# Performance work log

Measured on AMD Instinct MI355X. Metric: run time of the kernel, lower is better.

## Reference

```python
import jax, jax.numpy as jnp
import numpy as np
from jax import lax

S = 20      # max_segments
D = 1000    # traj_dict entries
L = 200     # dmp_traj_length
CONV_OUT = 512 * 4 * 4  # 8192 for 100x100 input


def _conv(x, w, b):
    # NCHW valid conv, kernel 3x3, stride 1 (matches nn.Conv2d defaults)
    y = lax.conv_general_dilated(x, w, (1, 1), 'VALID',
                                 dimension_numbers=('NCHW', 'OIHW', 'NCHW'))
    return y + b[None, :, None, None]


def _pool2(x):
    # max_pool2d(kernel=2, stride=2), floor mode == VALID reduce_window
    return lax.reduce_window(x, -jnp.inf, lax.max, (1, 1, 2, 2), (1, 1, 2, 2), 'VALID')


def setup_inputs() -> dict:
    key = jax.random.key(0)
    ks = jax.random.split(key, 20)
    f32 = jnp.float32

    def rn(k, shape, s):
        return jax.random.normal(k, shape, dtype=f32) * s

    x = jax.random.normal(ks[0], (128, 3, 100, 100), dtype=f32)
    w1 = rn(ks[1], (64, 3, 3, 3), 0.1);    b1 = jnp.zeros((64,), f32)
    w2 = rn(ks[2], (128, 64, 3, 3), 0.04); b2 = jnp.zeros((128,), f32)
    w3 = rn(ks[3], (256, 128, 3, 3), 0.03); b3 = jnp.zeros((256,), f32)
    w4 = rn(ks[4], (512, 256, 3, 3), 0.02); b4 = jnp.zeros((512,), f32)
    out_size = 2 + 3 * S
    fw1 = rn(ks[5], (CONV_OUT, 2048), 0.01); fb1 = jnp.zeros((2048,), f32)
    fw2 = rn(ks[6], (2048, 2048), 0.02);     fb2 = jnp.zeros((2048,), f32)
    fw3 = rn(ks[7], (2048, out_size), 0.02); fb3 = jnp.zeros((out_size,), f32)
    traj_dict = jax.random.normal(ks[8], (D, L, 2), dtype=f32)
    return {
        'x': x,
        'w1': w1, 'b1': b1, 'w2': w2, 'b2': b2,
        'w3': w3, 'b3': b3, 'w4': w4, 'b4': b4,
        'fw1': fw1, 'fb1': fb1, 'fw2': fw2, 'fb2': fb2,
        'fw3': fw3, 'fb3': fb3,
        'traj_dict': traj_dict,
    }


def _forward(x, w1, b1, w2, b2, w3, b3, w4, b4,
             fw1, fb1, fw2, fb2, fw3, fb3, traj_dict):
    # conv encoder (relu(maxpool(conv)) x4, matching the torch order)
    h = jax.nn.relu(_pool2(_conv(x, w1, b1)))
    h = jax.nn.relu(_pool2(_conv(h, w2, b2)))
    h = jax.nn.relu(_pool2(_conv(h, w3, b3)))
    h = jax.nn.relu(_pool2(_conv(h, w4, b4)))
    h = h.reshape(h.shape[0], -1)                      # [B, 8192]
    # FC stack: tanh on hidden layers, linear head (dropout p=0 / eval)
    h = jnp.tanh(h @ fw1 + fb1)
    h = jnp.tanh(h @ fw2 + fb2)
    p = h @ fw3 + fb3                                  # [B, 2 + 3S]

    B = p.shape[0]
    init_pos = p[:, :2]                                # [B, 2]
    seg = p[:, 2:].reshape(B, S, 3)                    # (dict_idx, x_scale, y_scale)

    # getTrajFromDict: the loop of round/clamp/sign/abs one-hot masks is exactly
    # a gather at the clamped rounded index (round is half-to-even in both torch and jax)
    idx = jnp.clip(jnp.round(seg[..., 0]), 0, D - 1).astype(jnp.int32)  # [B, S]
    base = traj_dict[idx]                              # [B, S, L, 2]

    scaled = base * seg[:, :, None, 1:3]               # [B, S, L, 2]
    # chain segments: each segment starts at previous segment's endpoint
    offsets = scaled[:, :, -1, :]                      # [B, S, 2]
    starts = init_pos[:, None, :] + jnp.cumsum(offsets, axis=1) - offsets  # exclusive cumsum
    traj = (scaled + starts[:, :, None, :]).reshape(B, S * L, 2)
    return traj


def reference(x, w1, b1, w2, b2, w3, b3, w4, b4,
              fw1, fb1, fw2, fb2, fw3, fb3, traj_dict):
    return _forward(x, w1, b1, w2, b2, w3, b3, w4, b4,
                    fw1, fb1, fw2, fb2, fw3, fb3, traj_dict)
```

## Files before the change

kernel.cpp:

```cpp
#include <hip/hip_runtime.h>
#include <hip/hip_bf16.h>

typedef __attribute__((ext_vector_type(8))) short s8v;
typedef __attribute__((ext_vector_type(4))) float f4v;
typedef unsigned short ushort;
typedef unsigned int uint;

union V8 { s8v v; short s[8]; };

__device__ __forceinline__ short f2bf(float v){
    union { __hip_bfloat16 b; short u; } x;
    x.b = __float2bfloat16(v);
    return x.u;
}
__device__ __forceinline__ float bf2f(short u){
    union { short u; __hip_bfloat16 b; } x;
    x.u = u;
    return __bfloat162float(x.b);
}
__device__ __forceinline__ void splitf(float v, short& h, short& l){
    h = f2bf(v);
    l = f2bf(v - bf2f(h));
}

__device__ __forceinline__ void gl_lds16(const void* g, void* l){
    __builtin_amdgcn_global_load_lds(
        (const __attribute__((address_space(1))) void*)g,
        (__attribute__((address_space(3))) void*)l, 16, 0, 0);
}

template<int CIN, int HIN, int PH, int OCB, int SPT, int CICH, int COUT>
__global__ __launch_bounds__(SPT) void k_conv_pool_relu(
    const float* __restrict__ in, const float* __restrict__ w,
    const float* __restrict__ bias, ushort* __restrict__ outh,
    ushort* __restrict__ outl)
{
    constexpr int WIN   = HIN;
    constexpr int PW    = PH;
    constexpr int WSTR  = CICH * 9 + 1;

    __shared__ float wsh[OCB * WSTR];

    const int b   = blockIdx.z;
    const int oc0 = blockIdx.y * OCB;
    const int t   = threadIdx.x;
    const int sp  = blockIdx.x * SPT + t;
    const bool active = sp < PH * PW;
    const int py = active ? (sp / PW) : 0;
    const int px = active ? (sp % PW) : 0;

    float acc[OCB][4];
#pragma unroll
    for (int j = 0; j < OCB; ++j)
        acc[j][0] = acc[j][1] = acc[j][2] = acc[j][3] = 0.f;

    const float* inb = in + (size_t)b * CIN * HIN * WIN;

    for (int c0 = 0; c0 < CIN; c0 += CICH) {
        __syncthreads();
        for (int i = t; i < OCB * CICH * 9; i += SPT) {
            int j = i / (CICH * 9);
            int r = i - j * (CICH * 9);
            wsh[j * WSTR + r] = w[((size_t)(oc0 + j) * CIN + c0) * 9 + r];
        }
        __syncthreads();

        for (int ci = 0; ci < CICH; ++ci) {
            const float* inc = inb + (size_t)(c0 + ci) * HIN * WIN
                             + (2 * py) * WIN + 2 * px;
            float patch[4][4];
#pragma unroll
            for (int r = 0; r < 4; ++r)
#pragma unroll
                for (int c = 0; c < 4; ++c)
                    patch[r][c] = inc[r * WIN + c];

#pragma unroll
            for (int j = 0; j < OCB; ++j) {
                const float* wp = &wsh[j * WSTR + ci * 9];
#pragma unroll
                for (int kh = 0; kh < 3; ++kh)
#pragma unroll
                    for (int kw = 0; kw < 3; ++kw) {
                        float wv = wp[kh * 3 + kw];
                        acc[j][0] = fmaf(patch[kh][kw],         wv, acc[j][0]);
                        acc[j][1] = fmaf(patch[kh][kw + 1],     wv, acc[j][1]);
                        acc[j][2] = fmaf(patch[kh + 1][kw],     wv, acc[j][2]);
                        acc[j][3] = fmaf(patch[kh + 1][kw + 1], wv, acc[j][3]);
                    }
            }
        }
    }

    if (active) {
        union { ushort us[OCB]; uint4 u4[OCB / 8]; } TH, TL;
#pragma unroll
        for (int j = 0; j < OCB; ++j) {
            float m = fmaxf(fmaxf(acc[j][0], acc[j][1]),
                            fmaxf(acc[j][2], acc[j][3]));
            m = fmaxf(m + bias[oc0 + j], 0.f);
            short h, l; splitf(m, h, l);
            TH.us[j] = (ushort)h; TL.us[j] = (ushort)l;
        }
        size_t base = ((size_t)b * PH * PW + sp) * COUT + oc0;
#pragma unroll
        for (int q = 0; q < OCB / 8; ++q) {
            ((uint4*)(outh + base))[q] = TH.u4[q];
            ((uint4*)(outl + base))[q] = TL.u4[q];
        }
    }
}

__global__ void k_wsplit_perm(const float* __restrict__ w, ushort* __restrict__ oh,
                              ushort* __restrict__ ol, int CIN, int total)
{
    int i = blockIdx.x * 256 + threadIdx.x;
    if (i < total) {
        int K = CIN * 9;
        int n = i / K;
        int rem = i - n * K;
        int ci = rem / 9;
        int r = rem - 9 * ci;
        short h, l; splitf(w[i], h, l);
        size_t o = (size_t)n * K + r * CIN + ci;
        oh[o] = (ushort)h; ol[o] = (ushort)l;
    }
}

__global__ __launch_bounds__(256) void k_wsplitT(
    const float* __restrict__ B, ushort* __restrict__ oh, ushort* __restrict__ ol,
    int K, int N)
{
    __shared__ float tl[32][33];
    const int n0 = blockIdx.x * 32, k0 = blockIdx.y * 32;
    const int r = threadIdx.x >> 5, c = threadIdx.x & 31;
#pragma unroll
    for (int it = 0; it < 4; ++it) {
        int row = r + it * 8;
        tl[row][c] = B[(size_t)(k0 + row) * N + n0 + c];
    }
    __syncthreads();
#pragma unroll
    for (int it = 0; it < 4; ++it) {
        int a = r + it * 8;
        float v = tl[c][a];
        short h, l; splitf(v, h, l);
        size_t o = (size_t)(n0 + a) * K + k0 + c;
        oh[o] = (ushort)h; ol[o] = (ushort)l;
    }
}

template<int MODE, int BPRE, int EPI, int LOG2CIN, int K, int KCH, int N,
         int HIN, int PPH, int PPW, int COUT, int TPI, int MT>
__global__ __launch_bounds__(256) void k_gemm4(
    const void* __restrict__ A0, const void* __restrict__ A1,
    const void* __restrict__ B0, const void* __restrict__ B1,
    const float* __restrict__ bias, void* __restrict__ O0, void* __restrict__ O1)
{
    constexpr int CIN  = 1 << LOG2CIN;
    constexpr int HH   = HIN * HIN;
    constexpr int WM   = MT / 32;
    constexpr int AOPT = MT / 64;
    constexpr int OSTEP = 256 / MT;

    __shared__ ushort Ah[4][MT][8], Al[4][MT][8];
    __shared__ ushort Bh[4][128][8], Bl[4][128][8];

    const int t    = threadIdx.x;
    const int lane = t & 63;
    const int wave = t >> 6;
    const int n0   = blockIdx.y * 128;
    const int sArow = t & (MT - 1), sAo0 = t / MT;
    const int sBrow = t & 127, sBo = t >> 7;
    const int rbA = sArow - lane;
    const int rbB = sBrow - lane;

    const ushort* Ahp = (const ushort*)A0;
    const ushort* Alp = (const ushort*)A1;
    size_t aoff = 0;
    const ushort* Ahg = nullptr;
    const ushort* Alg = nullptr;
    int b = 0, ptile = 0, kbeg = 0, kend = K;

    if (MODE == 0) {
        b = blockIdx.x / TPI;
        ptile = blockIdx.x - b * TPI;
        int pl = ptile * (MT / 4) + (sArow >> 2);
        int quad = sArow & 3;
        int py = 0, px = 0;
        if (pl < PPH * PPW) { py = pl / PPW; px = pl - py * PPW; }
        aoff = ((size_t)b * HH + (size_t)(2 * py + (quad >> 1)) * HIN
               + (2 * px + (quad & 1))) * CIN;
    } else {
        int arow = blockIdx.x * MT + sArow;
        Ahg = (const ushort*)A0 + (size_t)arow * K;
        Alg = (const ushort*)A1 + (size_t)arow * K;
        kbeg = blockIdx.z * KCH;
        kend = kbeg + KCH;
    }

    auto stage = [&](int kkx) {
#pragma unroll
        for (int q = 0; q < AOPT; ++q) {
            const int ko = sAo0 + q * OSTEP;
            const int kb = kkx + ko * 8;
            if (MODE == 0) {
                const int r  = kb >> LOG2CIN;
                const int cb = kb & (CIN - 1);
                const int rh = (r * 11) >> 5;
                const int rw = r - 3 * rh;
                const size_t g = aoff + (size_t)(rh * HIN + rw) * CIN + cb;
                gl_lds16(Ahp + g, &Ah[ko][rbA][0]);
                gl_lds16(Alp + g, &Al[ko][rbA][0]);
            } else {
                gl_lds16(Ahg + kb, &Ah[ko][rbA][0]);
                gl_lds16(Alg + kb, &Al[ko][rbA][0]);
            }
        }
        if (BPRE) {
#pragma unroll
            for (int q = 0; q < 2; ++q) {
                const int o = sBo + 2 * q;
                const int kb = kkx + o * 8;
                const size_t g = (size_t)(n0 + sBrow) * K + kb;
                gl_lds16((const ushort*)B0 + g, &Bh[o][rbB][0]);
                gl_lds16((const ushort*)B1 + g, &Bl[o][rbB][0]);
            }
        } else {
#pragma unroll
            for (int q = 0; q < 2; ++q) {
                const int o = sBo + 2 * q;
                const int kb = kkx + o * 8;
                V8 hb, lb;
                if (MODE == 0) {
                    const int r  = kb >> LOG2CIN;
                    const int cb = kb & (CIN - 1);
                    const float* bp = (const float*)B0
                        + (size_t)(n0 + sBrow) * K + (size_t)cb * 9 + r;
#pragma unroll
                    for (int j = 0; j < 8; ++j)
                        splitf(bp[9 * j], hb.s[j], lb.s[j]);
                } else {
                    const float* bp = (const float*)B0 + (size_t)kb * N + n0 + sBrow;
#pragma unroll
                    for (int j = 0; j < 8; ++j)
                        splitf(bp[(size_t)j * N], hb.s[j], lb.s[j]);
                }
                *(s8v*)&Bh[o][sBrow][0] = hb.v;
                *(s8v*)&Bl[o][sBrow][0] = lb.v;
            }
        }
    };

    f4v acc[WM][4];
    const f4v z4 = {0.f, 0.f, 0.f, 0.f};
#pragma unroll
    for (int i = 0; i < WM; ++i)
#pragma unroll
        for (int j = 0; j < 4; ++j) acc[i][j] = z4;

    for (int kk = kbeg; kk < kend; kk += 32) {
        stage(kk);
        __syncthreads();
        const int fm = lane & 15;
        const int ko = lane >> 4;
        s8v a_h[WM], a_l[WM], b_h[4], b_l[4];
#pragma unroll
        for (int i = 0; i < WM; ++i) {
            a_h[i] = *(const s8v*)&Ah[ko][(wave & 1) * (MT / 2) + i * 16 + fm][0];
            a_l[i] = *(const s8v*)&Al[ko][(wave & 1) * (MT / 2) + i * 16 + fm][0];
        }
#pragma unroll
        for (int j = 0; j < 4; ++j) {
            b_h[j] = *(const s8v*)&Bh[ko][(wave >> 1) * 64 + j * 16 + fm][0];
            b_l[j] = *(const s8v*)&Bl[ko][(wave >> 1) * 64 + j * 16 + fm][0];
        }
#define MF(a_, b_, c_) c_ = __builtin_amdgcn_mfma_f32_16x16x32_bf16(a_, b_, c_, 0, 0, 0)
#pragma unroll
        for (int i = 0; i < WM; ++i)
#pragma unroll
            for (int j = 0; j < 4; ++j) {
                MF(a_h[i], b_h[j], acc[i][j]);
                MF(a_h[i], b_l[j], acc[i][j]);
                MF(a_l[i], b_h[j], acc[i][j]);
            }
#undef MF
        __syncthreads();
    }

    if (MODE == 0) {
        const int PP = PPH * PPW;
#pragma unroll
        for (int i = 0; i < WM; ++i)
#pragma unroll
            for (int j = 0; j < 4; ++j) {
                int p  = ptile * (MT / 4) + (wave & 1) * (MT / 8) + i * 4 + (lane >> 4);
                int oc = n0 + (wave >> 1) * 64 + j * 16 + (lane & 15);
                if (p < PP) {
                    f4v v = acc[i][j];
                    float m = fmaxf(fmaxf(v.x, v.y), fmaxf(v.z, v.w));
                    m = fmaxf(m + bias[oc], 0.f);
                    short h, l; splitf(m, h, l);
                    if (EPI == 0) {
                        size_t o = ((size_t)b * PP + p) * COUT + oc;
                        ((ushort*)O0)[o] = (ushort)h;
                        ((ushort*)O1)[o] = (ushort)l;
                    } else {
                        size_t o = (size_t)(b * COUT + oc) * PP + p;
                        ((ushort*)O0)[o] = (ushort)h;
                        ((ushort*)O1)[o] = (ushort)l;
                    }
                }
            }
    } else {
        float* P = (float*)O0 + (size_t)blockIdx.z * 128 * N;
#pragma unroll
        for (int i = 0; i < WM; ++i)
#pragma unroll
            for (int j = 0; j < 4; ++j) {
                int n = n0 + (wave >> 1) * 64 + j * 16 + (lane & 15);
                int mb = blockIdx.x * MT + (wave & 1) * (MT / 2) + i * 16 + (lane >> 4) * 4;
                f4v v = acc[i][j];
                P[(size_t)(mb + 0) * N + n] = v.x;
                P[(size_t)(mb + 1) * N + n] = v.y;
                P[(size_t)(mb + 2) * N + n] = v.z;
                P[(size_t)(mb + 3) * N + n] = v.w;
            }
    }
}

template<int EFMT>
__global__ void k_fc_epi2(const float* __restrict__ P, const float* __restrict__ bias,
                          ushort* __restrict__ oh, ushort* __restrict__ ol,
                          float* __restrict__ of, int MN, int N, int KS)
{
    int i = blockIdx.x * 256 + threadIdx.x;
    if (i >= MN) return;
    float s = 0.f;
    for (int z = 0; z < KS; ++z) s += P[(size_t)z * MN + i];
    s = tanhf(s + bias[i % N]);
    if (EFMT == 1) {
        short h, l; splitf(s, h, l);
        oh[i] = (ushort)h; ol[i] = (ushort)l;
    } else {
        of[i] = s;
    }
}

__global__ __launch_bounds__(64) void k_fc3_part(
    const float* __restrict__ A, const float* __restrict__ B,
    float* __restrict__ P, int K, int N, int KS)
{
    const int m = blockIdx.x, kz = blockIdx.y;
    const int n = threadIdx.x;
    const int kchunk = K / KS;
    if (n < N) {
        float acc = 0.f;
        const float* Am = A + (size_t)m * K;
        const int ke = (kz + 1) * kchunk;
        for (int k = kz * kchunk; k < ke; ++k)
            acc = fmaf(Am[k], B[(size_t)k * N + n], acc);
        P[((size_t)kz * 128 + m) * N + n] = acc;
    }
}

__global__ void k_fc_epi(const float* __restrict__ P, const float* __restrict__ bias,
                         float* __restrict__ out, int MN, int N, int KS)
{
    int i = blockIdx.x * 256 + threadIdx.x;
    if (i >= MN) return;
    float s = 0.f;
    for (int z = 0; z < KS; ++z) s += P[(size_t)z * MN + i];
    out[i] = s + bias[i % N];
}

__global__ void k_traj_start(const float* __restrict__ p, const float* __restrict__ td,
                             float* __restrict__ starts, float* __restrict__ sa,
                             int* __restrict__ sidx)
{
    int b = threadIdx.x;
    const float* pb = p + b * 62;
    float cx = pb[0], cy = pb[1];
    for (int s = 0; s < 20; ++s) {
        float f  = pb[2 + 3 * s];
        float a0 = pb[3 + 3 * s];
        float a1 = pb[4 + 3 * s];
        int idx = (int)fminf(fmaxf(rintf(f), 0.f), 999.f);
        int bs = b * 20 + s;
        sidx[bs] = idx;
        sa[bs * 2 + 0] = a0;
        sa[bs * 2 + 1] = a1;
        starts[bs * 2 + 0] = cx;
        starts[bs * 2 + 1] = cy;
        cx += td[((size_t)idx * 200 + 199) * 2 + 0] * a0;
        cy += td[((size_t)idx * 200 + 199) * 2 + 1] * a1;
    }
}

__global__ void k_traj_main(const float* __restrict__ td, const float* __restrict__ starts,
                            const float* __restrict__ sa, const int* __restrict__ sidx,
                            float* __restrict__ out)
{
    int bs = blockIdx.x;
    int idx = sidx[bs];
    float a0 = sa[bs * 2 + 0], a1 = sa[bs * 2 + 1];
    float s0 = starts[bs * 2 + 0], s1 = starts[bs * 2 + 1];
    const float* row = td + (size_t)idx * 400;
    float* o = out + (size_t)bs * 400;
    for (int e = threadIdx.x; e < 400; e += blockDim.x) {
        float v = row[e];
        o[e] = (e & 1) ? fmaf(v, a1, s1) : fmaf(v, a0, s0);
    }
}

template<int BPRE>
static void run_all(void* const* d_in, float* out, char* ws, hipStream_t stream)
{
    const float* x   = (const float*)d_in[0];
    const float* w1  = (const float*)d_in[1];
    const float* b1  = (const float*)d_in[2];
    const float* w2  = (const float*)d_in[3];
    const float* b2  = (const float*)d_in[4];
    const float* w3  = (const float*)d_in[5];
    const float* b3  = (const float*)d_in[6];
    const float* w4  = (const float*)d_in[7];
    const float* b4  = (const float*)d_in[8];
    const float* fw1 = (const float*)d_in[9];
    const float* fb1 = (const float*)d_in[10];
    const float* fw2 = (const float*)d_in[11];
    const float* fb2 = (const float*)d_in[12];
    const float* fw3 = (const float*)d_in[13];
    const float* fb3 = (const float*)d_in[14];
    const float* td  = (const float*)d_in[15];

    ushort* h1h  = (ushort*)ws;
    ushort* h1l  = (ushort*)(ws + 39337984ull);
    ushort* h2h  = (ushort*)(ws + 78675968ull);
    ushort* h2l  = (ushort*)(ws + 96010240ull);
    ushort* h3h  = (ushort*)ws;
    ushort* h3l  = (ushort*)(ws + 6553600ull);
    ushort* fw1h = (ushort*)(ws + 13107200ull);
    ushort* fw1l = (ushort*)(ws + 46661632ull);
    ushort* h4h  = (ushort*)(ws + 80216064ull);
    ushort* h4l  = (ushort*)(ws + 82313216ull);
    ushort* fw2h = (ushort*)(ws + 84410368ull);
    ushort* fw2l = (ushort*)(ws + 92798976ull);
    float*  part = (float*)(ws + 101187584ull);
    ushort* a1h  = (ushort*)(ws + 109576192ull);
    ushort* a1l  = (ushort*)(ws + 110100480ull);
    float*  a2   = (float*)(ws + 110624768ull);
    float*  p    = (float*)(ws + 111673344ull);
    float*  starts = (float*)(ws + 111705088ull);
    float*  sa   = (float*)(ws + 111725568ull);
    int*    sidx = (int*)(ws + 111746048ull);
    ushort* w2h = (ushort*)(ws + 113344512ull);
    ushort* w2l = (ushort*)(ws + 113491968ull);
    ushort* w3h = (ushort*)(ws + 113639424ull);
    ushort* w3l = (ushort*)(ws + 114229248ull);
    ushort* w4h = (ushort*)(ws + 114819072ull);
    ushort* w4l = (ushort*)(ws + 117178368ull);

    if (BPRE) {
        k_wsplit_perm<<<(73728 + 255) / 256, 256, 0, stream>>>(w2, w2h, w2l, 64, 73728);
        k_wsplit_perm<<<(294912 + 255) / 256, 256, 0, stream>>>(w3, w3h, w3l, 128, 294912);
        k_wsplit_perm<<<(1179648 + 255) / 256, 256, 0, stream>>>(w4, w4h, w4l, 256, 1179648);
    }

    k_conv_pool_relu<3, 100, 49, 16, 256, 3, 64>
        <<<dim3(10, 4, 128), 256, 0, stream>>>(x, w1, b1, h1h, h1l);

    k_gemm4<0, BPRE, 0, 6, 576, 576, 128, 49, 23, 23, 128, 17, 128>
        <<<dim3(17 * 128, 1), 256, 0, stream>>>(
            h1h, h1l, BPRE ? (const void*)w2h : (const void*)w2,
            BPRE ? (const void*)w2l : nullptr, b2, h2h, h2l);
    k_gemm4<0, BPRE, 0, 7, 1152, 1152, 256, 23, 10, 10, 256, 4, 128>
        <<<dim3(4 * 128, 2), 256, 0, stream>>>(
            h2h, h2l, BPRE ? (const void*)w3h : (const void*)w3,
            BPRE ? (const void*)w3l : nullptr, b3, h3h, h3l);

    if (BPRE) {
        k_wsplitT<<<dim3(2048 / 32, 8192 / 32), 256, 0, stream>>>(fw1, fw1h, fw1l, 8192, 2048);
        k_wsplitT<<<dim3(2048 / 32, 2048 / 32), 256, 0, stream>>>(fw2, fw2h, fw2l, 2048, 2048);
    }

    k_gemm4<0, BPRE, 1, 8, 2304, 2304, 512, 10, 4, 4, 512, 1, 64>
        <<<dim3(128, 4), 256, 0, stream>>>(
            h3h, h3l, BPRE ? (const void*)w4h : (const void*)w4,
            BPRE ? (const void*)w4l : nullptr, b4, h4h, h4l);

    k_gemm4<1, BPRE, 2, 0, 8192, 1024, 2048, 1, 1, 1, 1, 1, 64>
        <<<dim3(2, 16, 8), 256, 0, stream>>>(
            h4h, h4l, BPRE ? (const void*)fw1h : (const void*)fw1,
            BPRE ? (const void*)fw1l : nullptr, nullptr, part, nullptr);
    k_fc_epi2<1><<<(128 * 2048 + 255) / 256, 256, 0, stream>>>(
        part, fb1, a1h, a1l, nullptr, 128 * 2048, 2048, 8);
    k_gemm4<1, BPRE, 2, 0, 2048, 256, 2048, 1, 1, 1, 1, 1, 64>
        <<<dim3(2, 16, 8), 256, 0, stream>>>(
            a1h, a1l, BPRE ? (const void*)fw2h : (const void*)fw2,
            BPRE ? (const void*)fw2l : nullptr, nullptr, part, nullptr);
    k_fc_epi2<2><<<(128 * 2048 + 255) / 256, 256, 0, stream>>>(
        part, fb2, nullptr, nullptr, a2, 128 * 2048, 2048, 8);

    k_fc3_part<<<dim3(128, 4), 64, 0, stream>>>(a2, fw3, part, 2048, 62, 4);
    k_fc_epi<<<(128 * 62 + 255) / 256, 256, 0, stream>>>(
        part, fb3, p, 128 * 62, 62, 4);
    k_traj_start<<<1, 128, 0, stream>>>(p, td, starts, sa, sidx);
    k_traj_main<<<2560, 256, 0, stream>>>(td, starts, sa, sidx, out);
}

extern "C" void kernel_launch(void* const* d_in, const int* in_sizes, int n_in,
                              void* d_out, int out_size, void* d_ws, size_t ws_size,
                              hipStream_t stream)
{
    (void)in_sizes; (void)n_in; (void)out_size;
    if (ws_size >= 119537664ull)
        run_all<1>(d_in, (float*)d_out, (char*)d_ws, stream);
    else
        run_all<0>(d_in, (float*)d_out, (char*)d_ws, stream);
}
```

Measured before the change: 1.000 ms.

## Double-buffer LDS tiles in the split-bf16 GEMM to overlap loads with MFMA

```diff
diff --git a/kernel.cpp b/kernel.cpp
--- a/kernel.cpp
+++ b/kernel.cpp
@@ -163,8 +163,8 @@
     constexpr int AOPT = MT / 64;
     constexpr int OSTEP = 256 / MT;
 
-    __shared__ ushort Ah[4][MT][8], Al[4][MT][8];
-    __shared__ ushort Bh[4][128][8], Bl[4][128][8];
+    __shared__ ushort Ah[2][4][MT][8], Al[2][4][MT][8];
+    __shared__ ushort Bh[2][4][128][8], Bl[2][4][128][8];
 
     const int t    = threadIdx.x;
     const int lane = t & 63;
@@ -199,7 +199,7 @@
         kend = kbeg + KCH;
     }
 
-    auto stage = [&](int kkx) {
+    auto stage = [&](int kkx, int buf) {
 #pragma unroll
         for (int q = 0; q < AOPT; ++q) {
             const int ko = sAo0 + q * OSTEP;
@@ -210,11 +210,11 @@
                 const int rh = (r * 11) >> 5;
                 const int rw = r - 3 * rh;
                 const size_t g = aoff + (size_t)(rh * HIN + rw) * CIN + cb;
-                gl_lds16(Ahp + g, &Ah[ko][rbA][0]);
-                gl_lds16(Alp + g, &Al[ko][rbA][0]);
+                gl_lds16(Ahp + g, &Ah[buf][ko][rbA][0]);
+                gl_lds16(Alp + g, &Al[buf][ko][rbA][0]);
             } else {
-                gl_lds16(Ahg + kb, &Ah[ko][rbA][0]);
-                gl_lds16(Alg + kb, &Al[ko][rbA][0]);
+                gl_lds16(Ahg + kb, &Ah[buf][ko][rbA][0]);
+                gl_lds16(Alg + kb, &Al[buf][ko][rbA][0]);
             }
         }
         if (BPRE) {
@@ -223,8 +223,8 @@
                 const int o = sBo + 2 * q;
                 const int kb = kkx + o * 8;
                 const size_t g = (size_t)(n0 + sBrow) * K + kb;
-                gl_lds16((const ushort*)B0 + g, &Bh[o][rbB][0]);
-                gl_lds16((const ushort*)B1 + g, &Bl[o][rbB][0]);
+                gl_lds16((const ushort*)B0 + g, &Bh[buf][o][rbB][0]);
+                gl_lds16((const ushort*)B1 + g, &Bl[buf][o][rbB][0]);
             }
         } else {
 #pragma unroll
@@ -246,8 +246,8 @@
                     for (int j = 0; j < 8; ++j)
                         splitf(bp[(size_t)j * N], hb.s[j], lb.s[j]);
                 }
-                *(s8v*)&Bh[o][sBrow][0] = hb.v;
-                *(s8v*)&Bl[o][sBrow][0] = lb.v;
+                *(s8v*)&Bh[buf][o][sBrow][0] = hb.v;
+                *(s8v*)&Bl[buf][o][sBrow][0] = lb.v;
             }
         }
     };
@@ -259,21 +259,25 @@
 #pragma unroll
         for (int j = 0; j < 4; ++j) acc[i][j] = z4;
 
+    stage(kbeg, 0);
+    __syncthreads();
+
+    int cur = 0;
     for (int kk = kbeg; kk < kend; kk += 32) {
-        stage(kk);
-        __syncthreads();
+        if (kk + 32 < kend)
+            stage(kk + 32, cur ^ 1);
         const int fm = lane & 15;
         const int ko = lane >> 4;
         s8v a_h[WM], a_l[WM], b_h[4], b_l[4];
 #pragma unroll
         for (int i = 0; i < WM; ++i) {
-            a_h[i] = *(const s8v*)&Ah[ko][(wave & 1) * (MT / 2) + i * 16 + fm][0];
-            a_l[i] = *(const s8v*)&Al[ko][(wave & 1) * (MT / 2) + i * 16 + fm][0];
+            a_h[i] = *(const s8v*)&Ah[cur][ko][(wave & 1) * (MT / 2) + i * 16 + fm][0];
+            a_l[i] = *(const s8v*)&Al[cur][ko][(wave & 1) * (MT / 2) + i * 16 + fm][0];
         }
 #pragma unroll
         for (int j = 0; j < 4; ++j) {
-            b_h[j] = *(const s8v*)&Bh[ko][(wave >> 1) * 64 + j * 16 + fm][0];
-            b_l[j] = *(const s8v*)&Bl[ko][(wave >> 1) * 64 + j * 16 + fm][0];
+            b_h[j] = *(const s8v*)&Bh[cur][ko][(wave >> 1) * 64 + j * 16 + fm][0];
+            b_l[j] = *(const s8v*)&Bl[cur][ko][(wave >> 1) * 64 + j * 16 + fm][0];
         }
 #define MF(a_, b_, c_) c_ = __builtin_amdgcn_mfma_f32_16x16x32_bf16(a_, b_, c_, 0, 0, 0)
 #pragma unroll
@@ -286,6 +290,7 @@
             }
 #undef MF
         __syncthreads();
+        cur ^= 1;
     }
 
     if (MODE == 0) {
```

Result: no change. 1.011 ms (+1.1%).
